# Optimization experiments

Measured on AMD Instinct MI355X. Metric: run time of the kernel, lower is better.

Reference implementation:

```python
import jax, jax.numpy as jnp
import numpy as np

N_TASKS, N_DATA, N_DEV = 200000, 100000, 4
E_TD, E_TT, E_DV = 800000, 1600000, 800000
D_TASK, D_DATA, D_DEVF = 12, 5, 12
DE_TD, DE_TT, DE_DV = 3, 1, 2
C = 64  # hidden_channels, n_heads=1, concat=False


def setup_inputs() -> dict:
    key = jax.random.key(0)
    ks = iter(jax.random.split(key, 64))
    nrm = lambda shape, s=1.0: jax.random.normal(next(ks), shape, dtype=jnp.float32) * s
    ridx = lambda n, hi: jax.random.randint(next(ks), (n,), 0, hi, dtype=jnp.int32)
    inp = {
        "x_tasks": nrm((N_TASKS, D_TASK)),
        "x_data": nrm((N_DATA, D_DATA)),
        "x_devices": nrm((N_DEV, D_DEVF)),
        "src_td": ridx(E_TD, N_DATA), "dst_td": ridx(E_TD, N_TASKS), "eattr_td": nrm((E_TD, DE_TD)),
        "src_tt": ridx(E_TT, N_TASKS), "dst_tt": ridx(E_TT, N_TASKS), "eattr_tt": nrm((E_TT, DE_TT)),
        "src_dv": ridx(E_DV, N_DEV), "dst_dv": ridx(E_DV, N_TASKS), "eattr_dv": nrm((E_DV, DE_DV)),
    }
    # GATConv parameters per relation (H=1): lin_src, lin_dst, lin_edge, att vectors, residual lin, bias
    for tag, ds, de in (("td", D_DATA, DE_TD), ("tt", D_TASK, DE_TT), ("dv", D_DEVF, DE_DV)):
        inp[f"Ws_{tag}"] = nrm((ds, C), 0.1)
        inp[f"Wd_{tag}"] = nrm((D_TASK, C), 0.1)
        inp[f"We_{tag}"] = nrm((de, C), 0.1)
        inp[f"as_{tag}"] = nrm((C,), 0.1)
        inp[f"ad_{tag}"] = nrm((C,), 0.1)
        inp[f"ae_{tag}"] = nrm((C,), 0.1)
        inp[f"Wr_{tag}"] = nrm((D_TASK, C), 0.1)
        inp[f"b_{tag}"] = jnp.zeros((C,), jnp.float32)
    inp["ln_g"] = jnp.ones((D_TASK + 3 * C,), jnp.float32)
    inp["ln_b"] = jnp.zeros((D_TASK + 3 * C,), jnp.float32)
    return inp


def _gat(x_src, x_dst, src, dst, eattr, Ws, Wd, We, a_s, a_d, a_e, Wr, b, n_dst):
    # PyG GATConv: heads=1, concat=False, residual=True, add_self_loops=False, edge_dim set
    hs = x_src @ Ws                       # [Ns, C]
    hd = x_dst @ Wd                       # [Nd, C]
    he = eattr @ We                       # [E, C]
    logits = (hs @ a_s)[src] + (hd @ a_d)[dst] + he @ a_e   # [E]
    logits = jax.nn.leaky_relu(logits, 0.2)
    m = jax.ops.segment_max(logits, dst, num_segments=n_dst)
    m = jnp.where(jnp.isfinite(m), m, 0.0)                  # empty segments -> 0
    ex = jnp.exp(logits - m[dst])
    denom = jax.ops.segment_sum(ex, dst, num_segments=n_dst)
    coef = ex / (denom[dst] + 1e-16)                        # segment softmax over incoming edges
    out = jax.ops.segment_sum(coef[:, None] * hs[src], dst, num_segments=n_dst)  # [Nd, C]
    return out + x_dst @ Wr + b                             # residual + bias


def reference(x_tasks, x_data, x_devices,
              src_td, dst_td, eattr_td, src_tt, dst_tt, eattr_tt, src_dv, dst_dv, eattr_dv,
              Ws_td, Wd_td, We_td, as_td, ad_td, ae_td, Wr_td, b_td,
              Ws_tt, Wd_tt, We_tt, as_tt, ad_tt, ae_tt, Wr_tt, b_tt,
              Ws_dv, Wd_dv, We_dv, as_dv, ad_dv, ae_dv, Wr_dv, b_dv,
              ln_g, ln_b):
    o_td = _gat(x_data, x_tasks, src_td, dst_td, eattr_td, Ws_td, Wd_td, We_td, as_td, ad_td, ae_td, Wr_td, b_td, N_TASKS)
    o_tt = _gat(x_tasks, x_tasks, src_tt, dst_tt, eattr_tt, Ws_tt, Wd_tt, We_tt, as_tt, ad_tt, ae_tt, Wr_tt, b_tt, N_TASKS)
    o_dv = _gat(x_devices, x_tasks, src_dv, dst_dv, eattr_dv, Ws_dv, Wd_dv, We_dv, as_dv, ad_dv, ae_dv, Wr_dv, b_dv, N_TASKS)
    # HeteroConv aggr='cat' over the 3 relations, then skip-concat of raw task features
    x = jnp.concatenate([x_tasks, o_td, o_tt, o_dv], axis=-1)  # [N_tasks, 12+3*64]
    mu = jnp.mean(x, axis=-1, keepdims=True)
    var = jnp.var(x, axis=-1, keepdims=True)
    x = (x - mu) * jax.lax.rsqrt(var + 1e-5) * ln_g + ln_b
    return jax.nn.leaky_relu(x, 0.01)
```

## Files before the change

kernel.cpp:

```cpp
#include <hip/hip_runtime.h>
#include <math.h>

#define N_TASKS 200000
#define N_DATA  100000
#define N_DEV   4
#define E_TD    800000
#define E_TT    1600000
#define E_DV    800000
#define E_ALL   (E_TD + E_TT + E_DV)

struct __align__(8) Payload { int src; float scal; };

#define OFF_HS_TD   0
#define OFF_HS_TT   (OFF_HS_TD + 6400000)
#define OFF_HS_DV   (OFF_HS_TT + 12800000)
#define OFF_SS_TD   (OFF_HS_DV + 256)
#define OFF_SS_TT   (OFF_SS_TD + 100000)
#define OFF_SS_DV   (OFF_SS_TT + 200000)
#define OFF_WDAD    (OFF_SS_DV + 8)
#define OFF_WEA     (OFF_WDAD + 64)
#define OFF_CNT     (OFF_WEA + 8)
#define OFF_PTR     (OFF_CNT + 600000)
#define OFF_AUX     (OFF_PTR + 600000)
#define OFF_PAY     (OFF_AUX + 1024)
#define SCAN_N      600000
#define SCAN_BLOCKS ((SCAN_N + 1023) / 1024)

#define HS_TD_B 25000
#define HS_TT_B 50000
#define CNT_B   12500
#define PRE_B   (HS_TD_B + HS_TT_B + 1 + CNT_B)

__global__ void prep_kernel(const float* Wd_td, const float* ad_td,
                            const float* Wd_tt, const float* ad_tt,
                            const float* Wd_dv, const float* ad_dv,
                            const float* We_td, const float* ae_td,
                            const float* We_tt, const float* ae_tt,
                            const float* We_dv, const float* ae_dv,
                            float* wdad, float* wea) {
    int t = threadIdx.x;
    if (t < 36) {
        int r = t / 12, k = t % 12;
        const float* Wd = r == 0 ? Wd_td : (r == 1 ? Wd_tt : Wd_dv);
        const float* ad = r == 0 ? ad_td : (r == 1 ? ad_tt : ad_dv);
        float acc = 0.f;
        for (int c = 0; c < 64; ++c) acc += Wd[k * 64 + c] * ad[c];
        wdad[r * 12 + k] = acc;
    } else if (t < 42) {
        int i = t - 36;
        int r, k;
        if (i < 3)      { r = 0; k = i; }
        else if (i < 4) { r = 1; k = 0; }
        else            { r = 2; k = i - 4; }
        const float* We = r == 0 ? We_td : (r == 1 ? We_tt : We_dv);
        const float* ae = r == 0 ? ae_td : (r == 1 ? ae_tt : ae_dv);
        float acc = 0.f;
        for (int c = 0; c < 64; ++c) acc += We[k * 64 + c] * ae[c];
        wea[i] = acc;
    }
}

__device__ __forceinline__ void hs_body(const float* __restrict__ x, int Ns, int ds,
                                        const float* __restrict__ Ws, const float* __restrict__ a_s,
                                        float* __restrict__ hs, float* __restrict__ ss,
                                        int blk, int tid) {
    int gid = blk * 256 + tid;
    int s = gid >> 6;
    int lane = gid & 63;
    if (s >= Ns) return;
    float acc = 0.f;
    for (int k = 0; k < ds; ++k) acc += x[(size_t)s * ds + k] * Ws[k * 64 + lane];
    hs[(size_t)s * 64 + lane] = acc;
    float t = acc * a_s[lane];
    for (int off = 32; off; off >>= 1) t += __shfl_down(t, off, 64);
    if (lane == 0) ss[s] = t;
}

__global__ __launch_bounds__(256) void pre_kernel(
    const float* __restrict__ x_data, const float* __restrict__ x_tasks, const float* __restrict__ x_devices,
    const float* __restrict__ Ws_td, const float* __restrict__ as_td,
    const float* __restrict__ Ws_tt, const float* __restrict__ as_tt,
    const float* __restrict__ Ws_dv, const float* __restrict__ as_dv,
    float* __restrict__ hs_td, float* __restrict__ ss_td,
    float* __restrict__ hs_tt, float* __restrict__ ss_tt,
    float* __restrict__ hs_dv, float* __restrict__ ss_dv,
    const int* __restrict__ dst_td, const int* __restrict__ dst_tt, const int* __restrict__ dst_dv,
    int* __restrict__ cnt) {
    int b = blockIdx.x, tid = threadIdx.x;
    if (b < HS_TD_B) { hs_body(x_data, N_DATA, 5, Ws_td, as_td, hs_td, ss_td, b, tid); return; }
    b -= HS_TD_B;
    if (b < HS_TT_B) { hs_body(x_tasks, N_TASKS, 12, Ws_tt, as_tt, hs_tt, ss_tt, b, tid); return; }
    b -= HS_TT_B;
    if (b == 0) { hs_body(x_devices, N_DEV, 12, Ws_dv, as_dv, hs_dv, ss_dv, 0, tid); return; }
    b -= 1;
    int i = b * 256 + tid;
    if (i < E_TD) {
        atomicAdd(&cnt[dst_td[i]], 1);
    } else if (i < E_TD + E_TT) {
        atomicAdd(&cnt[N_TASKS + dst_tt[i - E_TD]], 1);
    } else if (i < E_ALL) {
        atomicAdd(&cnt[2 * N_TASKS + dst_dv[i - E_TD - E_TT]], 1);
    }
}

__global__ void scan1(const int* __restrict__ cnt, int* __restrict__ ptr,
                      int* __restrict__ aux, int n) {
    __shared__ int s[256];
    int b = blockIdx.x, t = threadIdx.x;
    int base = b * 1024 + t * 4;
    int v0 = base + 0 < n ? cnt[base + 0] : 0;
    int v1 = base + 1 < n ? cnt[base + 1] : 0;
    int v2 = base + 2 < n ? cnt[base + 2] : 0;
    int v3 = base + 3 < n ? cnt[base + 3] : 0;
    int tsum = v0 + v1 + v2 + v3;
    s[t] = tsum;
    __syncthreads();
    for (int off = 1; off < 256; off <<= 1) {
        int x = (t >= off) ? s[t - off] : 0;
        __syncthreads();
        s[t] += x;
        __syncthreads();
    }
    int p = s[t] - tsum;
    if (t == 255) aux[b] = s[255];
    if (base + 0 < n) ptr[base + 0] = p; p += v0;
    if (base + 1 < n) ptr[base + 1] = p; p += v1;
    if (base + 2 < n) ptr[base + 2] = p; p += v2;
    if (base + 3 < n) ptr[base + 3] = p;
}

__global__ void scan2(int* __restrict__ aux, int nb) {
    __shared__ int s[256];
    int t = threadIdx.x;
    int carry = 0;
    for (int base = 0; base < nb; base += 256) {
        int i = base + t;
        int v = i < nb ? aux[i] : 0;
        s[t] = v;
        __syncthreads();
        for (int off = 1; off < 256; off <<= 1) {
            int x = (t >= off) ? s[t - off] : 0;
            __syncthreads();
            s[t] += x;
            __syncthreads();
        }
        int excl = s[t] - v + carry;
        if (i < nb) aux[i] = excl;
        int total = s[255];
        __syncthreads();
        carry += total;
    }
}

__global__ void scatter_all(const int* __restrict__ src_td, const int* __restrict__ dst_td, const float* __restrict__ ea_td,
                            const int* __restrict__ src_tt, const int* __restrict__ dst_tt, const float* __restrict__ ea_tt,
                            const int* __restrict__ src_dv, const int* __restrict__ dst_dv, const float* __restrict__ ea_dv,
                            const float* __restrict__ wea, const float* __restrict__ wdad,
                            const float* __restrict__ x_tasks,
                            const float* __restrict__ ss_td, const float* __restrict__ ss_tt, const float* __restrict__ ss_dv,
                            int* __restrict__ cursor, const int* __restrict__ aux,
                            Payload* __restrict__ payload) {
    int i = blockIdx.x * blockDim.x + threadIdx.x;
    if (i >= E_ALL) return;
    int s, dnode, r;
    float sc;
    if (i < E_TD) {
        int e = i;
        r = 0;
        sc = ea_td[(size_t)e * 3 + 0] * wea[0] + ea_td[(size_t)e * 3 + 1] * wea[1] + ea_td[(size_t)e * 3 + 2] * wea[2];
        s = src_td[e];
        sc += ss_td[s];
        dnode = dst_td[e];
    } else if (i < E_TD + E_TT) {
        int e = i - E_TD;
        r = 1;
        sc = ea_tt[e] * wea[3];
        s = src_tt[e];
        sc += ss_tt[s];
        dnode = dst_tt[e];
    } else {
        int e = i - E_TD - E_TT;
        r = 2;
        sc = ea_dv[(size_t)e * 2 + 0] * wea[4] + ea_dv[(size_t)e * 2 + 1] * wea[5];
        s = src_dv[e];
        sc += ss_dv[s];
        dnode = dst_dv[e];
    }
    const float4* xt4 = (const float4*)(x_tasks + (size_t)dnode * 12);
    float4 xa = xt4[0], xb = xt4[1], xc = xt4[2];
    const float* wd = wdad + r * 12;
    sc += xa.x * wd[0] + xa.y * wd[1] + xa.z * wd[2] + xa.w * wd[3]
        + xb.x * wd[4] + xb.y * wd[5] + xb.z * wd[6] + xb.w * wd[7]
        + xc.x * wd[8] + xc.y * wd[9] + xc.z * wd[10] + xc.w * wd[11];
    float lg = sc > 0.f ? sc : 0.2f * sc;
    int dseg = r * N_TASKS + dnode;
    int pos = atomicAdd(&cursor[dseg], 1) + aux[dseg >> 10];
    Payload p; p.src = s; p.scal = __expf(lg);
    payload[pos] = p;
}

__device__ __forceinline__ float gat_wave(
    int d, int r, int lane,
    const int* __restrict__ ptr, const int* __restrict__ cnt, const int* __restrict__ aux,
    const Payload* __restrict__ payload,
    const float* __restrict__ hs, const float* __restrict__ Wr, const float* __restrict__ bb,
    const float* __restrict__ xp) {
    int idx = r * N_TASKS + d;
    int end = ptr[idx] + aux[idx >> 10];
    int beg = end - cnt[idx];
    float acc = 0.f, wsum = 0.f;
    #pragma unroll 4
    for (int e = beg; e < end; ++e) {
        Payload p = payload[e];
        acc = fmaf(p.scal, hs[(size_t)p.src * 64 + lane], acc);
        wsum += p.scal;
    }
    float res = bb[lane];
    #pragma unroll
    for (int k = 0; k < 12; ++k) res = fmaf(xp[k], Wr[k * 64 + lane], res);
    return acc / (wsum + 1e-16f) + res;
}

__global__ __launch_bounds__(256) void fused_node_kernel(
    const float* __restrict__ x_tasks,
    const int* __restrict__ ptr, const int* __restrict__ cnt, const int* __restrict__ aux,
    const Payload* __restrict__ payload,
    const float* __restrict__ hs_td, const float* __restrict__ hs_tt, const float* __restrict__ hs_dv,
    const float* __restrict__ Wr_td, const float* __restrict__ Wr_tt, const float* __restrict__ Wr_dv,
    const float* __restrict__ b_td, const float* __restrict__ b_tt, const float* __restrict__ b_dv,
    const float* __restrict__ ln_g, const float* __restrict__ ln_b,
    float* __restrict__ out) {
    int wid = (blockIdx.x * blockDim.x + threadIdx.x) >> 6;
    if (wid >= N_TASKS) return;
    int d = __builtin_amdgcn_readfirstlane(wid);
    int lane = threadIdx.x & 63;

    const float* xp = x_tasks + (size_t)d * 12;
    float xl = lane < 12 ? xp[lane] : 0.f;

    float a0 = gat_wave(d, 0, lane, ptr, cnt, aux, payload, hs_td, Wr_td, b_td, xp);
    float a1 = gat_wave(d, 1, lane, ptr, cnt, aux, payload, hs_tt, Wr_tt, b_tt, xp);
    float a2 = gat_wave(d, 2, lane, ptr, cnt, aux, payload, hs_dv, Wr_dv, b_dv, xp);

    float sum = a0 + a1 + a2 + xl;
    float sq  = a0 * a0 + a1 * a1 + a2 * a2 + xl * xl;
    #pragma unroll
    for (int off = 1; off < 64; off <<= 1) {
        sum += __shfl_xor(sum, off, 64);
        sq  += __shfl_xor(sq, off, 64);
    }
    float mu = sum * (1.f / 204.f);
    float rstd = rsqrtf(sq * (1.f / 204.f) - mu * mu + 1e-5f);

    float* op = out + (size_t)d * 204;
    if (lane < 12) {
        float y = (xl - mu) * rstd * ln_g[lane] + ln_b[lane];
        op[lane] = y > 0.f ? y : 0.01f * y;
    }
    {
        float y = (a0 - mu) * rstd * ln_g[12 + lane] + ln_b[12 + lane];
        op[12 + lane] = y > 0.f ? y : 0.01f * y;
    }
    {
        float y = (a1 - mu) * rstd * ln_g[76 + lane] + ln_b[76 + lane];
        op[76 + lane] = y > 0.f ? y : 0.01f * y;
    }
    {
        float y = (a2 - mu) * rstd * ln_g[140 + lane] + ln_b[140 + lane];
        op[140 + lane] = y > 0.f ? y : 0.01f * y;
    }
}

extern "C" void kernel_launch(void* const* d_in, const int* in_sizes, int n_in,
                              void* d_out, int out_size, void* d_ws, size_t ws_size,
                              hipStream_t stream) {
    const float* x_tasks   = (const float*)d_in[0];
    const float* x_data    = (const float*)d_in[1];
    const float* x_devices = (const float*)d_in[2];
    const int*   src_td = (const int*)d_in[3];
    const int*   dst_td = (const int*)d_in[4];
    const float* eattr_td = (const float*)d_in[5];
    const int*   src_tt = (const int*)d_in[6];
    const int*   dst_tt = (const int*)d_in[7];
    const float* eattr_tt = (const float*)d_in[8];
    const int*   src_dv = (const int*)d_in[9];
    const int*   dst_dv = (const int*)d_in[10];
    const float* eattr_dv = (const float*)d_in[11];
    const float* Ws_td = (const float*)d_in[12];
    const float* Wd_td = (const float*)d_in[13];
    const float* We_td = (const float*)d_in[14];
    const float* as_td = (const float*)d_in[15];
    const float* ad_td = (const float*)d_in[16];
    const float* ae_td = (const float*)d_in[17];
    const float* Wr_td = (const float*)d_in[18];
    const float* b_td  = (const float*)d_in[19];
    const float* Ws_tt = (const float*)d_in[20];
    const float* Wd_tt = (const float*)d_in[21];
    const float* We_tt = (const float*)d_in[22];
    const float* as_tt = (const float*)d_in[23];
    const float* ad_tt = (const float*)d_in[24];
    const float* ae_tt = (const float*)d_in[25];
    const float* Wr_tt = (const float*)d_in[26];
    const float* b_tt  = (const float*)d_in[27];
    const float* Ws_dv = (const float*)d_in[28];
    const float* Wd_dv = (const float*)d_in[29];
    const float* We_dv = (const float*)d_in[30];
    const float* as_dv = (const float*)d_in[31];
    const float* ad_dv = (const float*)d_in[32];
    const float* ae_dv = (const float*)d_in[33];
    const float* Wr_dv = (const float*)d_in[34];
    const float* b_dv  = (const float*)d_in[35];
    const float* ln_g  = (const float*)d_in[36];
    const float* ln_b  = (const float*)d_in[37];

    float* ws = (float*)d_ws;
    float* hs_td = ws + OFF_HS_TD;
    float* hs_tt = ws + OFF_HS_TT;
    float* hs_dv = ws + OFF_HS_DV;
    float* ss_td = ws + OFF_SS_TD;
    float* ss_tt = ws + OFF_SS_TT;
    float* ss_dv = ws + OFF_SS_DV;
    float* wdad  = ws + OFF_WDAD;
    float* wea   = ws + OFF_WEA;
    int*   cnt   = (int*)(ws + OFF_CNT);
    int*   ptr   = (int*)(ws + OFF_PTR);
    int*   aux   = (int*)(ws + OFF_AUX);
    Payload* pay = (Payload*)(ws + OFF_PAY);

    float* outp = (float*)d_out;

    hipMemsetAsync(cnt, 0, SCAN_N * sizeof(int), stream);

    prep_kernel<<<1, 64, 0, stream>>>(Wd_td, ad_td, Wd_tt, ad_tt, Wd_dv, ad_dv,
                                      We_td, ae_td, We_tt, ae_tt, We_dv, ae_dv,
                                      wdad, wea);

    pre_kernel<<<PRE_B, 256, 0, stream>>>(
        x_data, x_tasks, x_devices,
        Ws_td, as_td, Ws_tt, as_tt, Ws_dv, as_dv,
        hs_td, ss_td, hs_tt, ss_tt, hs_dv, ss_dv,
        dst_td, dst_tt, dst_dv, cnt);

    scan1<<<SCAN_BLOCKS, 256, 0, stream>>>(cnt, ptr, aux, SCAN_N);
    scan2<<<1, 256, 0, stream>>>(aux, SCAN_BLOCKS);

    scatter_all<<<(E_ALL + 255) / 256, 256, 0, stream>>>(
        src_td, dst_td, eattr_td, src_tt, dst_tt, eattr_tt, src_dv, dst_dv, eattr_dv,
        wea, wdad, x_tasks, ss_td, ss_tt, ss_dv, ptr, aux, pay);

    fused_node_kernel<<<(N_TASKS * 64 + 255) / 256, 256, 0, stream>>>(
        x_tasks, ptr, cnt, aux, pay, hs_td, hs_tt, hs_dv,
        Wr_td, Wr_tt, Wr_dv, b_td, b_tt, b_dv, ln_g, ln_b, outp);
}
```

Measured before the change: 793.3 us.

## Move destination logit term and exp into node kernel; template hs_body

The destination-side attention term (x_dst·Wd·a_d) is no longer computed per edge in the scatter kernel, which had to gather 48 bytes of x_tasks for every edge. Each node wave now computes it once per relation and applies leaky-relu and exp per edge inside the aggregation loop. The scatter kernel stores raw partial logits instead. The hs projection is templated on input width with unrolled loads, and the count atomics are placed first in pre_kernel's block order. The cost is that exp is now computed redundantly by all 64 lanes of the wave for every edge.

```diff
diff --git a/kernel.cpp b/kernel.cpp
--- a/kernel.cpp
+++ b/kernel.cpp
@@ -26,10 +26,10 @@
 #define SCAN_N      600000
 #define SCAN_BLOCKS ((SCAN_N + 1023) / 1024)
 
+#define CNT_B   12500
 #define HS_TD_B 25000
 #define HS_TT_B 50000
-#define CNT_B   12500
-#define PRE_B   (HS_TD_B + HS_TT_B + 1 + CNT_B)
+#define PRE_B   (CNT_B + HS_TD_B + HS_TT_B + 1)
 
 __global__ void prep_kernel(const float* Wd_td, const float* ad_td,
                             const float* Wd_tt, const float* ad_tt,
@@ -60,7 +60,8 @@
     }
 }
 
-__device__ __forceinline__ void hs_body(const float* __restrict__ x, int Ns, int ds,
+template <int DS>
+__device__ __forceinline__ void hs_body(const float* __restrict__ x, int Ns,
                                         const float* __restrict__ Ws, const float* __restrict__ a_s,
                                         float* __restrict__ hs, float* __restrict__ ss,
                                         int blk, int tid) {
@@ -68,8 +69,12 @@
     int s = gid >> 6;
     int lane = gid & 63;
     if (s >= Ns) return;
+    float xv[DS];
+    #pragma unroll
+    for (int k = 0; k < DS; ++k) xv[k] = x[(size_t)s * DS + k];
     float acc = 0.f;
-    for (int k = 0; k < ds; ++k) acc += x[(size_t)s * ds + k] * Ws[k * 64 + lane];
+    #pragma unroll
+    for (int k = 0; k < DS; ++k) acc = fmaf(xv[k], Ws[k * 64 + lane], acc);
     hs[(size_t)s * 64 + lane] = acc;
     float t = acc * a_s[lane];
     for (int off = 32; off; off >>= 1) t += __shfl_down(t, off, 64);
@@ -87,20 +92,23 @@
     const int* __restrict__ dst_td, const int* __restrict__ dst_tt, const int* __restrict__ dst_dv,
     int* __restrict__ cnt) {
     int b = blockIdx.x, tid = threadIdx.x;
-    if (b < HS_TD_B) { hs_body(x_data, N_DATA, 5, Ws_td, as_td, hs_td, ss_td, b, tid); return; }
+    if (b < CNT_B) {
+        int i = b * 256 + tid;
+        if (i < E_TD) {
+            atomicAdd(&cnt[dst_td[i]], 1);
+        } else if (i < E_TD + E_TT) {
+            atomicAdd(&cnt[N_TASKS + dst_tt[i - E_TD]], 1);
+        } else if (i < E_ALL) {
+            atomicAdd(&cnt[2 * N_TASKS + dst_dv[i - E_TD - E_TT]], 1);
+        }
+        return;
+    }
+    b -= CNT_B;
+    if (b < HS_TD_B) { hs_body<5>(x_data, N_DATA, Ws_td, as_td, hs_td, ss_td, b, tid); return; }
     b -= HS_TD_B;
-    if (b < HS_TT_B) { hs_body(x_tasks, N_TASKS, 12, Ws_tt, as_tt, hs_tt, ss_tt, b, tid); return; }
+    if (b < HS_TT_B) { hs_body<12>(x_tasks, N_TASKS, Ws_tt, as_tt, hs_tt, ss_tt, b, tid); return; }
     b -= HS_TT_B;
-    if (b == 0) { hs_body(x_devices, N_DEV, 12, Ws_dv, as_dv, hs_dv, ss_dv, 0, tid); return; }
-    b -= 1;
-    int i = b * 256 + tid;
-    if (i < E_TD) {
-        atomicAdd(&cnt[dst_td[i]], 1);
-    } else if (i < E_TD + E_TT) {
-        atomicAdd(&cnt[N_TASKS + dst_tt[i - E_TD]], 1);
-    } else if (i < E_ALL) {
-        atomicAdd(&cnt[2 * N_TASKS + dst_dv[i - E_TD - E_TT]], 1);
-    }
+    hs_body<12>(x_devices, N_DEV, Ws_dv, as_dv, hs_dv, ss_dv, 0, tid);
 }
 
 __global__ void scan1(const int* __restrict__ cnt, int* __restrict__ ptr,
@@ -155,47 +163,35 @@
 __global__ void scatter_all(const int* __restrict__ src_td, const int* __restrict__ dst_td, const float* __restrict__ ea_td,
                             const int* __restrict__ src_tt, const int* __restrict__ dst_tt, const float* __restrict__ ea_tt,
                             const int* __restrict__ src_dv, const int* __restrict__ dst_dv, const float* __restrict__ ea_dv,
-                            const float* __restrict__ wea, const float* __restrict__ wdad,
-                            const float* __restrict__ x_tasks,
+                            const float* __restrict__ wea,
                             const float* __restrict__ ss_td, const float* __restrict__ ss_tt, const float* __restrict__ ss_dv,
                             int* __restrict__ cursor, const int* __restrict__ aux,
                             Payload* __restrict__ payload) {
     int i = blockIdx.x * blockDim.x + threadIdx.x;
     if (i >= E_ALL) return;
-    int s, dnode, r;
+    int s, dseg;
     float sc;
     if (i < E_TD) {
         int e = i;
-        r = 0;
         sc = ea_td[(size_t)e * 3 + 0] * wea[0] + ea_td[(size_t)e * 3 + 1] * wea[1] + ea_td[(size_t)e * 3 + 2] * wea[2];
         s = src_td[e];
         sc += ss_td[s];
-        dnode = dst_td[e];
+        dseg = dst_td[e];
     } else if (i < E_TD + E_TT) {
         int e = i - E_TD;
-        r = 1;
         sc = ea_tt[e] * wea[3];
         s = src_tt[e];
         sc += ss_tt[s];
-        dnode = dst_tt[e];
+        dseg = N_TASKS + dst_tt[e];
     } else {
         int e = i - E_TD - E_TT;
-        r = 2;
         sc = ea_dv[(size_t)e * 2 + 0] * wea[4] + ea_dv[(size_t)e * 2 + 1] * wea[5];
         s = src_dv[e];
         sc += ss_dv[s];
-        dnode = dst_dv[e];
-    }
-    const float4* xt4 = (const float4*)(x_tasks + (size_t)dnode * 12);
-    float4 xa = xt4[0], xb = xt4[1], xc = xt4[2];
-    const float* wd = wdad + r * 12;
-    sc += xa.x * wd[0] + xa.y * wd[1] + xa.z * wd[2] + xa.w * wd[3]
-        + xb.x * wd[4] + xb.y * wd[5] + xb.z * wd[6] + xb.w * wd[7]
-        + xc.x * wd[8] + xc.y * wd[9] + xc.z * wd[10] + xc.w * wd[11];
-    float lg = sc > 0.f ? sc : 0.2f * sc;
-    int dseg = r * N_TASKS + dnode;
+        dseg = 2 * N_TASKS + dst_dv[e];
+    }
     int pos = atomicAdd(&cursor[dseg], 1) + aux[dseg >> 10];
-    Payload p; p.src = s; p.scal = __expf(lg);
+    Payload p; p.src = s; p.scal = sc;
     payload[pos] = p;
 }
 
@@ -204,16 +200,22 @@
     const int* __restrict__ ptr, const int* __restrict__ cnt, const int* __restrict__ aux,
     const Payload* __restrict__ payload,
     const float* __restrict__ hs, const float* __restrict__ Wr, const float* __restrict__ bb,
-    const float* __restrict__ xp) {
+    const float* __restrict__ xp, const float* __restrict__ wdad) {
     int idx = r * N_TASKS + d;
     int end = ptr[idx] + aux[idx >> 10];
     int beg = end - cnt[idx];
+    float c = 0.f;
+    #pragma unroll
+    for (int k = 0; k < 12; ++k) c = fmaf(xp[k], wdad[r * 12 + k], c);
     float acc = 0.f, wsum = 0.f;
     #pragma unroll 4
     for (int e = beg; e < end; ++e) {
         Payload p = payload[e];
-        acc = fmaf(p.scal, hs[(size_t)p.src * 64 + lane], acc);
-        wsum += p.scal;
+        float sc = p.scal + c;
+        float lg = sc > 0.f ? sc : 0.2f * sc;
+        float w = __expf(lg);
+        acc = fmaf(w, hs[(size_t)p.src * 64 + lane], acc);
+        wsum += w;
     }
     float res = bb[lane];
     #pragma unroll
@@ -226,6 +228,7 @@
     const int* __restrict__ ptr, const int* __restrict__ cnt, const int* __restrict__ aux,
     const Payload* __restrict__ payload,
     const float* __restrict__ hs_td, const float* __restrict__ hs_tt, const float* __restrict__ hs_dv,
+    const float* __restrict__ wdad,
     const float* __restrict__ Wr_td, const float* __restrict__ Wr_tt, const float* __restrict__ Wr_dv,
     const float* __restrict__ b_td, const float* __restrict__ b_tt, const float* __restrict__ b_dv,
     const float* __restrict__ ln_g, const float* __restrict__ ln_b,
@@ -238,9 +241,9 @@
     const float* xp = x_tasks + (size_t)d * 12;
     float xl = lane < 12 ? xp[lane] : 0.f;
 
-    float a0 = gat_wave(d, 0, lane, ptr, cnt, aux, payload, hs_td, Wr_td, b_td, xp);
-    float a1 = gat_wave(d, 1, lane, ptr, cnt, aux, payload, hs_tt, Wr_tt, b_tt, xp);
-    float a2 = gat_wave(d, 2, lane, ptr, cnt, aux, payload, hs_dv, Wr_dv, b_dv, xp);
+    float a0 = gat_wave(d, 0, lane, ptr, cnt, aux, payload, hs_td, Wr_td, b_td, xp, wdad);
+    float a1 = gat_wave(d, 1, lane, ptr, cnt, aux, payload, hs_tt, Wr_tt, b_tt, xp, wdad);
+    float a2 = gat_wave(d, 2, lane, ptr, cnt, aux, payload, hs_dv, Wr_dv, b_dv, xp, wdad);
 
     float sum = a0 + a1 + a2 + xl;
     float sq  = a0 * a0 + a1 * a1 + a2 * a2 + xl * xl;
@@ -346,9 +349,9 @@
 
     scatter_all<<<(E_ALL + 255) / 256, 256, 0, stream>>>(
         src_td, dst_td, eattr_td, src_tt, dst_tt, eattr_tt, src_dv, dst_dv, eattr_dv,
-        wea, wdad, x_tasks, ss_td, ss_tt, ss_dv, ptr, aux, pay);
+        wea, ss_td, ss_tt, ss_dv, ptr, aux, pay);
 
     fused_node_kernel<<<(N_TASKS * 64 + 255) / 256, 256, 0, stream>>>(
-        x_tasks, ptr, cnt, aux, pay, hs_td, hs_tt, hs_dv,
+        x_tasks, ptr, cnt, aux, pay, hs_td, hs_tt, hs_dv, wdad,
         Wr_td, Wr_tt, Wr_dv, b_td, b_tt, b_dv, ln_g, ln_b, outp);
 }
```

After: 794.1 us. Within noise of the previous version (+0.1%).
